# Optimization experiments

Hardware: AMD Instinct MI355X
Metric: run time of the kernel (lower is better)

The kernel has to match this reference:

```python
import jax, jax.numpy as jnp
import numpy as np

N_NODES = 10000
N_EDGES = 320000
IN_DIM = 256
DIM = 256
HID = 256
OUT_DIM = 64
LAYERS = 4
NEG_SLOPE = 0.2


def setup_inputs() -> dict:
    key = jax.random.key(0)
    ks = jax.random.split(key, 12)
    s = 0.05
    return {
        "x": jax.random.normal(ks[0], (N_NODES, IN_DIM), jnp.float32),
        "edge_index": jax.random.randint(ks[1], (2, N_EDGES), 0, N_NODES, jnp.int64),
        "lin1_w": jax.random.normal(ks[2], (IN_DIM, DIM), jnp.float32) * s,
        "lin1_b": jnp.zeros((DIM,), jnp.float32),
        "gat_w": jax.random.normal(ks[3], (LAYERS, DIM, DIM), jnp.float32) * s,
        "gat_asrc": jax.random.normal(ks[4], (LAYERS, DIM), jnp.float32) * s,
        "gat_adst": jax.random.normal(ks[5], (LAYERS, DIM), jnp.float32) * s,
        "gat_b": jnp.zeros((LAYERS, DIM), jnp.float32),
        "lstm_wih": jax.random.normal(ks[6], (LAYERS, 4 * HID, 2 * DIM), jnp.float32) * s,
        "lstm_whh": jax.random.normal(ks[7], (LAYERS, 4 * HID, HID), jnp.float32) * s,
        "lin2_w": jax.random.normal(ks[8], (DIM, OUT_DIM), jnp.float32) * s,
        "lin2_b": jnp.zeros((OUT_DIM,), jnp.float32),
    }


def _gat_layer(x, src, dst, n, W, a_src, a_dst, b):
    # PyG GATConv (heads=1, concat=True): project, edge attention, scatter-softmax over dst
    xw = x @ W                                   # [N, D]
    a_s = xw @ a_src                             # [N]
    a_d = xw @ a_dst                             # [N]
    alpha = a_s[src] + a_d[dst]                  # [E]
    alpha = jnp.where(alpha > 0, alpha, NEG_SLOPE * alpha)  # leaky_relu
    m = jax.ops.segment_max(alpha, dst, num_segments=n)
    e = jnp.exp(alpha - m[dst])
    denom = jax.ops.segment_sum(e, dst, num_segments=n)
    coef = e / denom[dst]                        # softmax over edges sharing dst
    out = jax.ops.segment_sum(coef[:, None] * xw[src], dst, num_segments=n)
    return out + b


def reference(x, edge_index, lin1_w, lin1_b, gat_w, gat_asrc, gat_adst, gat_b,
              lstm_wih, lstm_whh, lin2_w, lin2_b):
    n = x.shape[0]
    # add self loops (GATConv default)
    loops = jnp.arange(n, dtype=edge_index.dtype)
    src = jnp.concatenate([edge_index[0], loops])
    dst = jnp.concatenate([edge_index[1], loops])

    x0 = x @ lin1_w + lin1_b                     # [N, DIM]
    h_tmps = [jnp.tanh(_gat_layer(x0, src, dst, n, gat_w[i], gat_asrc[i], gat_adst[i], gat_b[i]))
              for i in range(LAYERS)]

    h = jnp.zeros((n, HID), x0.dtype)
    c = jnp.zeros((n, HID), x0.dtype)
    xc = x0
    for i in range(LAYERS):
        inp = jnp.concatenate([h_tmps[i], xc], axis=-1)          # [N, 2*DIM]
        gates = inp @ lstm_wih[i].T + h @ lstm_whh[i].T          # [N, 4*HID]
        ig, fg, gg, og = jnp.split(gates, 4, axis=-1)            # torch gate order i,f,g,o
        c = jax.nn.sigmoid(fg) * c + jax.nn.sigmoid(ig) * jnp.tanh(gg)
        h = jax.nn.sigmoid(og) * jnp.tanh(c)
        xc = h
    return xc @ lin2_w + lin2_b
```

## Files before the change

kernel.cpp:

```cpp
#include <hip/hip_runtime.h>
#include <hip/hip_bf16.h>
#include <math.h>

#define N_NODES 10000
#define E_RAW   320000
#define E_TOT   330000
#define DIM     256
#define HID     256
#define OUTD    64
#define LAYERS  4

typedef short    short8 __attribute__((ext_vector_type(8)));
typedef float    f32x4  __attribute__((ext_vector_type(4)));
typedef _Float16 h4v    __attribute__((ext_vector_type(4)));

__device__ __forceinline__ ushort f2bf(float f) {
    union { float f; unsigned u; } v; v.f = f;
    unsigned r = v.u + 0x7FFF + ((v.u >> 16) & 1);
    return (ushort)(r >> 16);
}
__device__ __forceinline__ float bf2f(ushort h) {
    union { unsigned u; float f; } v; v.u = ((unsigned)h) << 16;
    return v.f;
}
__device__ __forceinline__ void split_bf(float f, ushort& hi, ushort& lo) {
    hi = f2bf(f);
    lo = f2bf(f - bf2f(hi));
}

__device__ __forceinline__ void gload16(const void* g, void* l) {
    __builtin_amdgcn_global_load_lds(
        (const __attribute__((address_space(1))) unsigned int*)g,
        (__attribute__((address_space(3))) unsigned int*)l,
        16, 0, 0);
}

__global__ void edge_hist(const int* __restrict__ ei, int* __restrict__ deg) {
    int e = blockIdx.x * blockDim.x + threadIdx.x;
    if (e >= E_TOT) return;
    int d = (e < E_RAW) ? ei[E_RAW + e] : (e - E_RAW);
    atomicAdd(&deg[d], 1);
}

__global__ __launch_bounds__(1024) void scan_deg(const int* __restrict__ deg,
                                                 int* __restrict__ row_start) {
    __shared__ int ps[1024];
    int t = threadIdx.x;
    int begin = t * 10;
    int end   = begin + 10; if (end > N_NODES) end = N_NODES;
    int s = 0;
    for (int i = begin; i < end; ++i) s += deg[i];
    ps[t] = s;
    __syncthreads();
    for (int off = 1; off < 1024; off <<= 1) {
        int v = (t >= off) ? ps[t - off] : 0;
        __syncthreads();
        ps[t] += v;
        __syncthreads();
    }
    int excl = (t == 0) ? 0 : ps[t - 1];
    for (int i = begin; i < end; ++i) {
        row_start[i] = excl;
        excl += deg[i];
    }
    if (t == 1023) row_start[N_NODES] = ps[1023];
}

__global__ void edge_scatter(const int* __restrict__ ei, const int* __restrict__ row_start,
                             int* __restrict__ cursor, int* __restrict__ ssrc) {
    int e = blockIdx.x * blockDim.x + threadIdx.x;
    if (e >= E_TOT) return;
    int s, d;
    if (e < E_RAW) { s = ei[e]; d = ei[E_RAW + e]; }
    else           { s = e - E_RAW; d = s; }
    int pos = row_start[d] + atomicAdd(&cursor[d], 1);
    ssrc[pos] = s;
}

__global__ void split_lstm_w(const float* __restrict__ wih, const float* __restrict__ whh,
                             ushort* __restrict__ wh, ushort* __restrict__ wl) {
    int gid = blockIdx.x * blockDim.x + threadIdx.x;
    if (gid >= LAYERS * 1024 * 512 / 4) return;
    int i4  = gid * 4;
    int l   = i4 / (1024 * 512);
    int rem = i4 - l * (1024 * 512);
    int R   = rem / 512;
    int k   = rem - R * 512;
    float4 v = *reinterpret_cast<const float4*>(wih + ((size_t)(l * 1024 + R) * 512) + k);
    if (l > 0 && k >= 256) {
        float4 w2 = *reinterpret_cast<const float4*>(whh + ((size_t)(l * 1024 + R) * 256) + (k - 256));
        v.x += w2.x; v.y += w2.y; v.z += w2.z; v.w += w2.w;
    }
    int gate = R >> 8, hu = R & 255;
    int gp = ((hu >> 4) << 6) + (gate << 4) + (hu & 15);
    ushort4 h4, l4;
    split_bf(v.x, h4.x, l4.x); split_bf(v.y, h4.y, l4.y);
    split_bf(v.z, h4.z, l4.z); split_bf(v.w, h4.w, l4.w);
    size_t dst = (size_t)(l * 1024 + gp) * 512 + k;
    *reinterpret_cast<ushort4*>(wh + dst) = h4;
    *reinterpret_cast<ushort4*>(wl + dst) = l4;
}

__global__ void split_gat_w(const float* __restrict__ gat_w,
                            ushort* __restrict__ gh, ushort* __restrict__ gl) {
    int gid = blockIdx.x * blockDim.x + threadIdx.x;
    if (gid >= LAYERS * 256 * 64) return;
    int l   = gid >> 14;
    int rem = gid & 16383;
    int n   = rem >> 6;
    int k4  = (rem & 63) * 4;
    ushort4 h4, l4;
    float v0 = gat_w[((size_t)l * 256 + k4 + 0) * 256 + n];
    float v1 = gat_w[((size_t)l * 256 + k4 + 1) * 256 + n];
    float v2 = gat_w[((size_t)l * 256 + k4 + 2) * 256 + n];
    float v3 = gat_w[((size_t)l * 256 + k4 + 3) * 256 + n];
    split_bf(v0, h4.x, l4.x); split_bf(v1, h4.y, l4.y);
    split_bf(v2, h4.z, l4.z); split_bf(v3, h4.w, l4.w);
    size_t dst = ((size_t)l * 256 + n) * 256 + k4;
    *reinterpret_cast<ushort4*>(gh + dst) = h4;
    *reinterpret_cast<ushort4*>(gl + dst) = l4;
}

__global__ void split_wT(const float* __restrict__ w, ushort* __restrict__ oh,
                         ushort* __restrict__ ol, int K, int N) {
    int gid = blockIdx.x * blockDim.x + threadIdx.x;
    if (gid >= N * K) return;
    int n = gid / K, k = gid - n * K;
    ushort hi, lo;
    split_bf(w[(size_t)k * N + n], hi, lo);
    oh[gid] = hi; ol[gid] = lo;
}

__global__ void split_x(const float* __restrict__ x, ushort* __restrict__ xh,
                        ushort* __restrict__ xl, int total4) {
    int gid = blockIdx.x * blockDim.x + threadIdx.x;
    if (gid >= total4) return;
    float4 v = *reinterpret_cast<const float4*>(x + (size_t)gid * 4);
    ushort4 h4, l4;
    split_bf(v.x, h4.x, l4.x); split_bf(v.y, h4.y, l4.y);
    split_bf(v.z, h4.z, l4.z); split_bf(v.w, h4.w, l4.w);
    *reinterpret_cast<ushort4*>(xh + (size_t)gid * 4) = h4;
    *reinterpret_cast<ushort4*>(xl + (size_t)gid * 4) = l4;
}

__global__ __launch_bounds__(256, 2) void gemm_bf3(
        const ushort* __restrict__ Ah0, const ushort* __restrict__ Al0,
        const ushort* __restrict__ Ah1, const ushort* __restrict__ Al1,
        const ushort* __restrict__ Bh,  const ushort* __restrict__ Bl,
        const float* __restrict__ bias,
        float* __restrict__ C, ushort* __restrict__ Oh, ushort* __restrict__ Ol,
        _Float16* __restrict__ Xh, float* __restrict__ Cc,
        int M, int N, int K, int mode) {
    __shared__ ushort lds[16384];

    int tid  = threadIdx.x;
    int lane = tid & 63;
    int w    = tid >> 6;
    int wm   = w >> 1, wn = w & 1;

    int gx = gridDim.x;
    int nwg = gx * gridDim.y;
    int orig = blockIdx.y * gx + blockIdx.x;
    int q8 = nwg >> 3, r7 = nwg & 7;
    int xcd = orig & 7, rest = orig >> 3;
    int wg = (xcd < r7 ? xcd * (q8 + 1) : r7 * (q8 + 1) + (xcd - r7) * q8) + rest;
    int bm = (wg % gx) * 128, bn = (wg / gx) * 128;

    f32x4 acc[4][4];
#pragma unroll
    for (int i = 0; i < 4; ++i)
#pragma unroll
        for (int j = 0; j < 4; ++j)
#pragma unroll
            for (int qq = 0; qq < 4; ++qq) acc[i][j][qq] = 0.f;

    int l15 = lane & 15;
    int skg = (lane >> 4) * 8;

    for (int k0 = 0; k0 < K; k0 += 32) {
        const ushort* gs;
        if (w == 0)      gs = (k0 < 256) ? Ah0 : Ah1;
        else if (w == 1) gs = (k0 < 256) ? Al0 : Al1;
        else if (w == 2) gs = Bh;
        else             gs = Bl;
        int    rowbase = (w < 2) ? bm : bn;
        size_t rstride = (w < 2) ? 256 : (size_t)K;
        int    kk      = (w < 2) ? ((k0 & 255) + skg) : (k0 + skg);
#pragma unroll
        for (int blk = 0; blk < 8; ++blk) {
            const ushort* g = gs + (size_t)(rowbase + blk * 16 + l15) * rstride + kk;
            int lidx = __builtin_amdgcn_readfirstlane(w * 4096 + blk * 512);
            gload16(g, (void*)&lds[lidx]);
        }
        __syncthreads();

        short8 afh[4], afl[4], bfh[4], bfl[4];
#pragma unroll
        for (int i = 0; i < 4; ++i) {
            afh[i] = *reinterpret_cast<const short8*>(&lds[        (wm * 4 + i) * 512 + lane * 8]);
            afl[i] = *reinterpret_cast<const short8*>(&lds[ 4096 + (wm * 4 + i) * 512 + lane * 8]);
            bfh[i] = *reinterpret_cast<const short8*>(&lds[ 8192 + (wn * 4 + i) * 512 + lane * 8]);
            bfl[i] = *reinterpret_cast<const short8*>(&lds[12288 + (wn * 4 + i) * 512 + lane * 8]);
        }
#pragma unroll
        for (int i = 0; i < 4; ++i)
#pragma unroll
            for (int j = 0; j < 4; ++j)
                acc[i][j] = __builtin_amdgcn_mfma_f32_16x16x32_bf16(afh[i], bfh[j], acc[i][j], 0, 0, 0);
#pragma unroll
        for (int i = 0; i < 4; ++i)
#pragma unroll
            for (int j = 0; j < 4; ++j)
                acc[i][j] = __builtin_amdgcn_mfma_f32_16x16x32_bf16(afh[i], bfl[j], acc[i][j], 0, 0, 0);
#pragma unroll
        for (int i = 0; i < 4; ++i)
#pragma unroll
            for (int j = 0; j < 4; ++j)
                acc[i][j] = __builtin_amdgcn_mfma_f32_16x16x32_bf16(afl[i], bfh[j], acc[i][j], 0, 0, 0);
        __syncthreads();
    }

    if (mode == 3) {
        int hu = (((bn + wn * 64) >> 6) << 4) + l15;
#pragma unroll
        for (int i = 0; i < 4; ++i) {
#pragma unroll
            for (int rr = 0; rr < 4; ++rr) {
                int n = bm + wm * 64 + i * 16 + (lane >> 4) * 4 + rr;
                if (n >= M) continue;
                float ig = acc[i][0][rr], fg = acc[i][1][rr];
                float gg = acc[i][2][rr], og = acc[i][3][rr];
                float si = 1.f / (1.f + expf(-ig));
                float sf = 1.f / (1.f + expf(-fg));
                float so = 1.f / (1.f + expf(-og));
                size_t o = (size_t)n * 256 + hu;
                float cn = sf * Cc[o] + si * tanhf(gg);
                float hn = so * tanhf(cn);
                Cc[o] = cn;
                ushort hi2, lo2; split_bf(hn, hi2, lo2);
                Oh[o] = hi2; Ol[o] = lo2;
            }
        }
        return;
    }
#pragma unroll
    for (int i = 0; i < 4; ++i) {
        int row0 = bm + wm * 64 + i * 16 + (lane >> 4) * 4;
#pragma unroll
        for (int j = 0; j < 4; ++j) {
            int col = bn + wn * 64 + j * 16 + l15;
            if (col >= N) continue;
            float bs = bias ? bias[col] : 0.f;
#pragma unroll
            for (int rr = 0; rr < 4; ++rr) {
                int row = row0 + rr;
                if (row >= M) continue;
                float o = acc[i][j][rr] + bs;
                if (mode == 0) {
                    C[(size_t)row * N + col] = o;
                } else if (mode == 1) {
                    Xh[((size_t)(col >> 8) * M + row) * 256 + (col & 255)] = (_Float16)o;
                } else {
                    ushort hi, lo; split_bf(o, hi, lo);
                    Oh[(size_t)row * N + col] = hi;
                    Ol[(size_t)row * N + col] = lo;
                }
            }
        }
    }
}

__global__ void compute_asd(const _Float16* __restrict__ xw_all,
                            const float* __restrict__ asrc_all,
                            const float* __restrict__ adst_all,
                            float* __restrict__ a_s, float* __restrict__ a_d) {
    int gt = blockIdx.x * blockDim.x + threadIdx.x;
    int gw = gt >> 6, lane = gt & 63;
    if (gw >= LAYERS * N_NODES) return;
    int l = gw / N_NODES;
    h4v v = *reinterpret_cast<const h4v*>(xw_all + (size_t)gw * 256 + lane * 4);
    float4 sa = *reinterpret_cast<const float4*>(asrc_all + l * 256 + lane * 4);
    float4 da = *reinterpret_cast<const float4*>(adst_all + l * 256 + lane * 4);
    float v0 = (float)v[0], v1 = (float)v[1], v2 = (float)v[2], v3 = (float)v[3];
    float s = v0*sa.x + v1*sa.y + v2*sa.z + v3*sa.w;
    float d = v0*da.x + v1*da.y + v2*da.z + v3*da.w;
    for (int off = 32; off; off >>= 1) {
        s += __shfl_down(s, off);
        d += __shfl_down(d, off);
    }
    if (lane == 0) { a_s[gw] = s; a_d[gw] = d; }
}

__global__ __launch_bounds__(256) void gat_aggregate(const _Float16* __restrict__ xw_all,
                                                     const float* __restrict__ a_s,
                                                     const float* __restrict__ a_d,
                                                     const int* __restrict__ row_start,
                                                     const int* __restrict__ ssrc,
                                                     const float* __restrict__ gat_b,
                                                     ushort* __restrict__ htmph,
                                                     ushort* __restrict__ htmpl) {
    int gw = blockIdx.x * 4 + (threadIdx.x >> 6);
    if (gw >= LAYERS * N_NODES) return;
    int l = gw / N_NODES, n = gw - l * N_NODES;
    int lane = threadIdx.x & 63;
    int beg = row_start[n], end = row_start[n + 1];
    const _Float16* xw = xw_all + (size_t)l * N_NODES * 256;
    const float* asl = a_s + (size_t)l * N_NODES;
    float adn = a_d[gw];

    float lm = -3.4e38f;
    for (int e = beg + lane; e < end; e += 64) {
        float s = asl[ssrc[e]] + adn;
        s = (s > 0.f) ? s : 0.2f * s;
        lm = fmaxf(lm, s);
    }
    for (int off = 32; off; off >>= 1) lm = fmaxf(lm, __shfl_xor(lm, off));
    float m = lm;

    float ls = 0.f;
    for (int e = beg + lane; e < end; e += 64) {
        float s = asl[ssrc[e]] + adn;
        s = (s > 0.f) ? s : 0.2f * s;
        ls += expf(s - m);
    }
    for (int off = 32; off; off >>= 1) ls += __shfl_xor(ls, off);
    float inv = 1.f / ls;

    float4 acc = make_float4(0.f, 0.f, 0.f, 0.f);
    for (int ch = beg; ch < end; ch += 64) {
        int e = ch + lane;
        float cfo = 0.f; int s0o = 0;
        if (e < end) {
            s0o = ssrc[e];
            float s = asl[s0o] + adn;
            s = (s > 0.f) ? s : 0.2f * s;
            cfo = expf(s - m) * inv;
        }
        int len = end - ch; if (len > 64) len = 64;
        for (int j = 0; j < len; ++j) {
            float cf = __shfl(cfo, j);
            int   s0 = __shfl(s0o, j);
            h4v v = *reinterpret_cast<const h4v*>(xw + (size_t)s0 * 256 + lane * 4);
            acc.x += cf * (float)v[0]; acc.y += cf * (float)v[1];
            acc.z += cf * (float)v[2]; acc.w += cf * (float)v[3];
        }
    }
    float4 b = *reinterpret_cast<const float4*>(gat_b + l * 256 + lane * 4);
    ushort4 h4, l4;
    split_bf(tanhf(acc.x + b.x), h4.x, l4.x);
    split_bf(tanhf(acc.y + b.y), h4.y, l4.y);
    split_bf(tanhf(acc.z + b.z), h4.z, l4.z);
    split_bf(tanhf(acc.w + b.w), h4.w, l4.w);
    size_t dst = (size_t)gw * 256 + lane * 4;
    *reinterpret_cast<ushort4*>(htmph + dst) = h4;
    *reinterpret_cast<ushort4*>(htmpl + dst) = l4;
}

extern "C" void kernel_launch(void* const* d_in, const int* in_sizes, int n_in,
                              void* d_out, int out_size, void* d_ws, size_t ws_size,
                              hipStream_t stream) {
    const float* x        = (const float*)d_in[0];
    const int*   ei       = (const int*)  d_in[1];
    const float* lin1_w   = (const float*)d_in[2];
    const float* lin1_b   = (const float*)d_in[3];
    const float* gat_w    = (const float*)d_in[4];
    const float* gat_asrc = (const float*)d_in[5];
    const float* gat_adst = (const float*)d_in[6];
    const float* gat_b    = (const float*)d_in[7];
    const float* lstm_wih = (const float*)d_in[8];
    const float* lstm_whh = (const float*)d_in[9];
    const float* lin2_w   = (const float*)d_in[10];
    const float* lin2_b   = (const float*)d_in[11];
    float* out = (float*)d_out;

    size_t off = 0;
    auto alloc = [&](size_t bytes) -> void* {
        void* p = (char*)d_ws + off;
        off = (off + bytes + 255) & ~(size_t)255;
        return p;
    };
    ushort* xh     = (ushort*)alloc((size_t)N_NODES * DIM * 2);
    ushort* xl     = (ushort*)alloc((size_t)N_NODES * DIM * 2);
    ushort* x0h    = (ushort*)alloc((size_t)N_NODES * DIM * 2);
    ushort* x0l    = (ushort*)alloc((size_t)N_NODES * DIM * 2);
    _Float16* xwh  = (_Float16*)alloc((size_t)LAYERS * N_NODES * DIM * 2);
    ushort* htmph  = (ushort*)alloc((size_t)LAYERS * N_NODES * DIM * 2);
    ushort* htmpl  = (ushort*)alloc((size_t)LAYERS * N_NODES * DIM * 2);
    float*  c      = (float*) alloc((size_t)N_NODES * HID * 4);
    ushort* hbh[2], *hbl[2];
    hbh[0] = (ushort*)alloc((size_t)N_NODES * HID * 2);
    hbl[0] = (ushort*)alloc((size_t)N_NODES * HID * 2);
    hbh[1] = (ushort*)alloc((size_t)N_NODES * HID * 2);
    hbl[1] = (ushort*)alloc((size_t)N_NODES * HID * 2);
    float*  a_s    = (float*) alloc((size_t)LAYERS * N_NODES * 4);
    float*  a_d    = (float*) alloc((size_t)LAYERS * N_NODES * 4);
    int* row_start = (int*)   alloc((size_t)(N_NODES + 1) * 4);
    int* cursor    = (int*)   alloc((size_t)N_NODES * 4);
    int* ssrc      = (int*)   alloc((size_t)E_TOT * 4);
    ushort* wlh    = (ushort*)alloc((size_t)LAYERS * 1024 * 512 * 2);
    ushort* wll    = (ushort*)alloc((size_t)LAYERS * 1024 * 512 * 2);
    ushort* gwh    = (ushort*)alloc((size_t)LAYERS * 256 * 256 * 2);
    ushort* gwl    = (ushort*)alloc((size_t)LAYERS * 256 * 256 * 2);
    ushort* l1h    = (ushort*)alloc((size_t)256 * 256 * 2);
    ushort* l1l    = (ushort*)alloc((size_t)256 * 256 * 2);
    ushort* l2h    = (ushort*)alloc((size_t)128 * 256 * 2);
    ushort* l2l    = (ushort*)alloc((size_t)128 * 256 * 2);
    (void)alloc(65536);

    hipMemsetAsync(cursor, 0, N_NODES * 4, stream);
    edge_hist<<<(E_TOT + 255) / 256, 256, 0, stream>>>(ei, cursor);
    scan_deg<<<1, 1024, 0, stream>>>(cursor, row_start);
    hipMemsetAsync(cursor, 0, N_NODES * 4, stream);
    edge_scatter<<<(E_TOT + 255) / 256, 256, 0, stream>>>(ei, row_start, cursor, ssrc);

    split_x<<<(N_NODES * DIM / 4 + 255) / 256, 256, 0, stream>>>(x, xh, xl, N_NODES * DIM / 4);
    split_lstm_w<<<(LAYERS * 1024 * 512 / 4 + 255) / 256, 256, 0, stream>>>(lstm_wih, lstm_whh, wlh, wll);
    split_gat_w<<<(LAYERS * 256 * 64 + 255) / 256, 256, 0, stream>>>(gat_w, gwh, gwl);
    split_wT<<<(256 * 256 + 255) / 256, 256, 0, stream>>>(lin1_w, l1h, l1l, 256, 256);
    split_wT<<<(64 * 256 + 255) / 256, 256, 0, stream>>>(lin2_w, l2h, l2l, 256, 64);

    hipMemsetAsync(c, 0, (size_t)N_NODES * HID * 4, stream);

    {
        dim3 grid((N_NODES + 127) / 128, 256 / 128);
        gemm_bf3<<<grid, 256, 0, stream>>>(xh, xl, xh, xl,
                                           l1h, l1l, lin1_b,
                                           nullptr, x0h, x0l, nullptr, nullptr,
                                           N_NODES, 256, 256, 2);
    }

    {
        dim3 grid((N_NODES + 127) / 128, (LAYERS * DIM) / 128);
        gemm_bf3<<<grid, 256, 0, stream>>>(x0h, x0l, x0h, x0l,
                                           gwh, gwl, nullptr,
                                           nullptr, nullptr, nullptr, xwh, nullptr,
                                           N_NODES, LAYERS * DIM, 256, 1);
        int waves = LAYERS * N_NODES;
        compute_asd<<<(waves * 64 + 255) / 256, 256, 0, stream>>>(xwh, gat_asrc, gat_adst,
                                                                  a_s, a_d);
        gat_aggregate<<<(waves + 3) / 4, 256, 0, stream>>>(xwh, a_s, a_d, row_start, ssrc,
                                                           gat_b, htmph, htmpl);
    }

    for (int l = 0; l < LAYERS; ++l) {
        const ushort* xch = (l == 0) ? x0h : hbh[(l - 1) & 1];
        const ushort* xcl = (l == 0) ? x0l : hbl[(l - 1) & 1];
        dim3 gridL((N_NODES + 127) / 128, 1024 / 128);
        gemm_bf3<<<gridL, 256, 0, stream>>>(
            htmph + (size_t)l * N_NODES * DIM, htmpl + (size_t)l * N_NODES * DIM,
            xch, xcl,
            wlh + (size_t)l * 1024 * 512, wll + (size_t)l * 1024 * 512,
            nullptr, nullptr, hbh[l & 1], hbl[l & 1], nullptr, c,
            N_NODES, 1024, 512, 3);
    }

    {
        dim3 grid((N_NODES + 127) / 128, 1);
        gemm_bf3<<<grid, 256, 0, stream>>>(hbh[1], hbl[1], hbh[1], hbl[1],
                                           l2h, l2l, lin2_b,
                                           out, nullptr, nullptr, nullptr, nullptr,
                                           N_NODES, OUTD, 256, 0);
    }
}
```

Baseline: 595.8 us.

## Store GEMM operands in MFMA-fragment blocked layout and drop XCD remapping

All bf16 hi/lo operand buffers (x, x0, GAT weights, LSTM weights, linear weights, htmp, h) are now written in a tiled layout of 16-row by 32-column blocks matching the LDS fragment order. Each wave's global-to-LDS load then reads one contiguous 1 KB chunk instead of 16 strided row segments. Row buffers are padded to 10112 rows so tail tiles read in-bounds memory, and one h buffer is zeroed for the padding. The XCD-aware workgroup remapping is removed in favour of plain blockIdx tiling, which may hurt L2 locality across chiplets. The scattered 2-byte epilogue writes into the blocked layout may also be less coalesced.

```diff
diff --git a/kernel.cpp b/kernel.cpp
--- a/kernel.cpp
+++ b/kernel.cpp
@@ -3,6 +3,7 @@
 #include <math.h>
 
 #define N_NODES 10000
+#define N_PAD   10112
 #define E_RAW   320000
 #define E_TOT   330000
 #define DIM     256
@@ -13,6 +14,11 @@
 typedef short    short8 __attribute__((ext_vector_type(8)));
 typedef float    f32x4  __attribute__((ext_vector_type(4)));
 typedef _Float16 h4v    __attribute__((ext_vector_type(4)));
+
+__host__ __device__ __forceinline__ size_t blk_off(int row, int col, int KC) {
+    return (((size_t)(row >> 4) * KC + (col >> 5)) * 64
+            + ((col >> 3) & 3) * 16 + (row & 15)) * 8 + (col & 7);
+}
 
 __device__ __forceinline__ ushort f2bf(float f) {
     union { float f; unsigned u; } v; v.f = f;
@@ -96,7 +102,7 @@
     ushort4 h4, l4;
     split_bf(v.x, h4.x, l4.x); split_bf(v.y, h4.y, l4.y);
     split_bf(v.z, h4.z, l4.z); split_bf(v.w, h4.w, l4.w);
-    size_t dst = (size_t)(l * 1024 + gp) * 512 + k;
+    size_t dst = (size_t)l * (1024 * 512) + blk_off(gp, k, 16);
     *reinterpret_cast<ushort4*>(wh + dst) = h4;
     *reinterpret_cast<ushort4*>(wl + dst) = l4;
 }
@@ -116,7 +122,7 @@
     float v3 = gat_w[((size_t)l * 256 + k4 + 3) * 256 + n];
     split_bf(v0, h4.x, l4.x); split_bf(v1, h4.y, l4.y);
     split_bf(v2, h4.z, l4.z); split_bf(v3, h4.w, l4.w);
-    size_t dst = ((size_t)l * 256 + n) * 256 + k4;
+    size_t dst = (size_t)l * (256 * 256) + blk_off(n, k4, 8);
     *reinterpret_cast<ushort4*>(gh + dst) = h4;
     *reinterpret_cast<ushort4*>(gl + dst) = l4;
 }
@@ -128,19 +134,22 @@
     int n = gid / K, k = gid - n * K;
     ushort hi, lo;
     split_bf(w[(size_t)k * N + n], hi, lo);
-    oh[gid] = hi; ol[gid] = lo;
+    size_t dst = blk_off(n, k, 8);
+    oh[dst] = hi; ol[dst] = lo;
 }
 
 __global__ void split_x(const float* __restrict__ x, ushort* __restrict__ xh,
                         ushort* __restrict__ xl, int total4) {
     int gid = blockIdx.x * blockDim.x + threadIdx.x;
     if (gid >= total4) return;
-    float4 v = *reinterpret_cast<const float4*>(x + (size_t)gid * 4);
+    int row = gid >> 6, c4 = (gid & 63) * 4;
+    float4 v = *reinterpret_cast<const float4*>(x + (size_t)row * 256 + c4);
     ushort4 h4, l4;
     split_bf(v.x, h4.x, l4.x); split_bf(v.y, h4.y, l4.y);
     split_bf(v.z, h4.z, l4.z); split_bf(v.w, h4.w, l4.w);
-    *reinterpret_cast<ushort4*>(xh + (size_t)gid * 4) = h4;
-    *reinterpret_cast<ushort4*>(xl + (size_t)gid * 4) = l4;
+    size_t dst = blk_off(row, c4, 8);
+    *reinterpret_cast<ushort4*>(xh + dst) = h4;
+    *reinterpret_cast<ushort4*>(xl + dst) = l4;
 }
 
 __global__ __launch_bounds__(256, 2) void gemm_bf3(
@@ -157,14 +166,7 @@
     int lane = tid & 63;
     int w    = tid >> 6;
     int wm   = w >> 1, wn = w & 1;
-
-    int gx = gridDim.x;
-    int nwg = gx * gridDim.y;
-    int orig = blockIdx.y * gx + blockIdx.x;
-    int q8 = nwg >> 3, r7 = nwg & 7;
-    int xcd = orig & 7, rest = orig >> 3;
-    int wg = (xcd < r7 ? xcd * (q8 + 1) : r7 * (q8 + 1) + (xcd - r7) * q8) + rest;
-    int bm = (wg % gx) * 128, bn = (wg / gx) * 128;
+    int bm = blockIdx.x * 128, bn = blockIdx.y * 128;
 
     f32x4 acc[4][4];
 #pragma unroll
@@ -175,20 +177,22 @@
             for (int qq = 0; qq < 4; ++qq) acc[i][j][qq] = 0.f;
 
     int l15 = lane & 15;
-    int skg = (lane >> 4) * 8;
+    int KCb = K >> 5;
 
     for (int k0 = 0; k0 < K; k0 += 32) {
         const ushort* gs;
-        if (w == 0)      gs = (k0 < 256) ? Ah0 : Ah1;
-        else if (w == 1) gs = (k0 < 256) ? Al0 : Al1;
-        else if (w == 2) gs = Bh;
-        else             gs = Bl;
-        int    rowbase = (w < 2) ? bm : bn;
-        size_t rstride = (w < 2) ? 256 : (size_t)K;
-        int    kk      = (w < 2) ? ((k0 & 255) + skg) : (k0 + skg);
+        size_t boff;
+        if (w < 2) {
+            gs = (k0 < 256) ? (w == 0 ? Ah0 : Al0) : (w == 0 ? Ah1 : Al1);
+            boff = (((size_t)(bm >> 4) * 8 + ((k0 & 255) >> 5)) * 64 + lane) * 8;
+        } else {
+            gs = (w == 2) ? Bh : Bl;
+            boff = (((size_t)(bn >> 4) * KCb + (k0 >> 5)) * 64 + lane) * 8;
+        }
+        size_t bstride = (w < 2) ? (8 * 512) : ((size_t)KCb * 512);
 #pragma unroll
         for (int blk = 0; blk < 8; ++blk) {
-            const ushort* g = gs + (size_t)(rowbase + blk * 16 + l15) * rstride + kk;
+            const ushort* g = gs + boff + (size_t)blk * bstride;
             int lidx = __builtin_amdgcn_readfirstlane(w * 4096 + blk * 512);
             gload16(g, (void*)&lds[lidx]);
         }
@@ -238,7 +242,8 @@
                 float hn = so * tanhf(cn);
                 Cc[o] = cn;
                 ushort hi2, lo2; split_bf(hn, hi2, lo2);
-                Oh[o] = hi2; Ol[o] = lo2;
+                size_t ob = blk_off(n, hu, 8);
+                Oh[ob] = hi2; Ol[ob] = lo2;
             }
         }
         return;
@@ -262,8 +267,9 @@
                     Xh[((size_t)(col >> 8) * M + row) * 256 + (col & 255)] = (_Float16)o;
                 } else {
                     ushort hi, lo; split_bf(o, hi, lo);
-                    Oh[(size_t)row * N + col] = hi;
-                    Ol[(size_t)row * N + col] = lo;
+                    size_t ob = blk_off(row, col, 8);
+                    Oh[ob] = hi;
+                    Ol[ob] = lo;
                 }
             }
         }
@@ -351,7 +357,7 @@
     split_bf(tanhf(acc.y + b.y), h4.y, l4.y);
     split_bf(tanhf(acc.z + b.z), h4.z, l4.z);
     split_bf(tanhf(acc.w + b.w), h4.w, l4.w);
-    size_t dst = (size_t)gw * 256 + lane * 4;
+    size_t dst = (size_t)l * ((size_t)N_PAD * 256) + blk_off(n, lane * 4, 8);
     *reinterpret_cast<ushort4*>(htmph + dst) = h4;
     *reinterpret_cast<ushort4*>(htmpl + dst) = l4;
 }
@@ -379,19 +385,19 @@
         off = (off + bytes + 255) & ~(size_t)255;
         return p;
     };
-    ushort* xh     = (ushort*)alloc((size_t)N_NODES * DIM * 2);
-    ushort* xl     = (ushort*)alloc((size_t)N_NODES * DIM * 2);
-    ushort* x0h    = (ushort*)alloc((size_t)N_NODES * DIM * 2);
-    ushort* x0l    = (ushort*)alloc((size_t)N_NODES * DIM * 2);
+    ushort* xh     = (ushort*)alloc((size_t)N_PAD * DIM * 2);
+    ushort* xl     = (ushort*)alloc((size_t)N_PAD * DIM * 2);
+    ushort* x0h    = (ushort*)alloc((size_t)N_PAD * DIM * 2);
+    ushort* x0l    = (ushort*)alloc((size_t)N_PAD * DIM * 2);
     _Float16* xwh  = (_Float16*)alloc((size_t)LAYERS * N_NODES * DIM * 2);
-    ushort* htmph  = (ushort*)alloc((size_t)LAYERS * N_NODES * DIM * 2);
-    ushort* htmpl  = (ushort*)alloc((size_t)LAYERS * N_NODES * DIM * 2);
+    ushort* htmph  = (ushort*)alloc((size_t)LAYERS * N_PAD * DIM * 2);
+    ushort* htmpl  = (ushort*)alloc((size_t)LAYERS * N_PAD * DIM * 2);
     float*  c      = (float*) alloc((size_t)N_NODES * HID * 4);
     ushort* hbh[2], *hbl[2];
-    hbh[0] = (ushort*)alloc((size_t)N_NODES * HID * 2);
-    hbl[0] = (ushort*)alloc((size_t)N_NODES * HID * 2);
-    hbh[1] = (ushort*)alloc((size_t)N_NODES * HID * 2);
-    hbl[1] = (ushort*)alloc((size_t)N_NODES * HID * 2);
+    hbh[0] = (ushort*)alloc((size_t)N_PAD * HID * 2);
+    hbl[0] = (ushort*)alloc((size_t)N_PAD * HID * 2);
+    hbh[1] = (ushort*)alloc((size_t)N_PAD * HID * 2);
+    hbl[1] = (ushort*)alloc((size_t)N_PAD * HID * 2);
     float*  a_s    = (float*) alloc((size_t)LAYERS * N_NODES * 4);
     float*  a_d    = (float*) alloc((size_t)LAYERS * N_NODES * 4);
     int* row_start = (int*)   alloc((size_t)(N_NODES + 1) * 4);
@@ -413,13 +419,15 @@
     hipMemsetAsync(cursor, 0, N_NODES * 4, stream);
     edge_scatter<<<(E_TOT + 255) / 256, 256, 0, stream>>>(ei, row_start, cursor, ssrc);
 
-    split_x<<<(N_NODES * DIM / 4 + 255) / 256, 256, 0, stream>>>(x, xh, xl, N_NODES * DIM / 4);
+    split_x<<<(N_NODES * 64 + 255) / 256, 256, 0, stream>>>(x, xh, xl, N_NODES * 64);
     split_lstm_w<<<(LAYERS * 1024 * 512 / 4 + 255) / 256, 256, 0, stream>>>(lstm_wih, lstm_whh, wlh, wll);
     split_gat_w<<<(LAYERS * 256 * 64 + 255) / 256, 256, 0, stream>>>(gat_w, gwh, gwl);
     split_wT<<<(256 * 256 + 255) / 256, 256, 0, stream>>>(lin1_w, l1h, l1l, 256, 256);
     split_wT<<<(64 * 256 + 255) / 256, 256, 0, stream>>>(lin2_w, l2h, l2l, 256, 64);
 
     hipMemsetAsync(c, 0, (size_t)N_NODES * HID * 4, stream);
+    hipMemsetAsync(hbh[1], 0, (size_t)N_PAD * HID * 2, stream);
+    hipMemsetAsync(hbl[1], 0, (size_t)N_PAD * HID * 2, stream);
 
     {
         dim3 grid((N_NODES + 127) / 128, 256 / 128);
@@ -447,7 +455,7 @@
         const ushort* xcl = (l == 0) ? x0l : hbl[(l - 1) & 1];
         dim3 gridL((N_NODES + 127) / 128, 1024 / 128);
         gemm_bf3<<<gridL, 256, 0, stream>>>(
-            htmph + (size_t)l * N_NODES * DIM, htmpl + (size_t)l * N_NODES * DIM,
+            htmph + (size_t)l * N_PAD * DIM, htmpl + (size_t)l * N_PAD * DIM,
             xch, xcl,
             wlh + (size_t)l * 1024 * 512, wll + (size_t)l * 1024 * 512,
             nullptr, nullptr, hbh[l & 1], hbl[l & 1], nullptr, c,
```

After: 529.8 us. -11.1%, faster.
